# Kernel tuning notes

Hardware: AMD Instinct MI355X
Metric: run time of the kernel (lower is better)

Reference implementation:

```python
import jax, jax.numpy as jnp
import numpy as np

LAMBDA = 20.0   # lambda_val (blackbox-diff smoothing)
REG = 0.5       # reg
MAX_LABEL = 8   # labels drawn in [0, MAX_LABEL)


def _pairwise_dist(x):
    # x: [n, d] -> [n, n] euclidean distances (safe sqrt, exact 0 on diagonal)
    sq = jnp.sum(x * x, axis=-1)
    d2 = sq[:, None] + sq[None, :] - 2.0 * (x @ x.T)
    d2 = jnp.maximum(d2, 0.0)
    return jnp.where(d2 > 0, jnp.sqrt(jnp.where(d2 > 0, d2, 1.0)), 0.0)


def _single_linkage_adj(D, k):
    # Agglomerative (single-linkage) clustering of n points given [n,n] dists,
    # stopped at k clusters; returns [n,n] 0/1 cluster-adjacency matrix.
    n = D.shape[0]
    BIG = jnp.asarray(1e9, D.dtype)
    eye = jnp.eye(n, dtype=bool)
    Dw0 = jnp.where(eye, BIG, D)
    labels0 = jnp.arange(n)
    active0 = jnp.ones((n,), dtype=bool)

    def step(carry, _):
        Dw, labels, active = carry
        mask = active[:, None] & active[None, :] & ~eye
        flat = jnp.argmin(jnp.where(mask, Dw, BIG))
        i, j = flat // n, flat % n
        a = jnp.minimum(i, j)
        b = jnp.maximum(i, j)
        newrow = jnp.minimum(Dw[a], Dw[b])        # single linkage merge
        Dw = Dw.at[a, :].set(newrow).at[:, a].set(newrow)
        active = active.at[b].set(False)
        labels = jnp.where(labels == b, a, labels)
        return (Dw, labels, active), labels

    _, hist = jax.lax.scan(step, (Dw0, labels0, active0), None, length=n - 1)
    all_hist = jnp.concatenate([labels0[None, :], hist], axis=0)  # [n, n]; row m = labels after m merges (n-m clusters)
    lab = all_hist[n - k]
    return (lab[:, None] == lab[None, :]).astype(D.dtype)


def _solve(dists, ks):
    return jax.vmap(_single_linkage_adj)(dists, ks)


def setup_inputs() -> dict:
    key = jax.random.key(0)
    k1, k2, k3 = jax.random.split(key, 3)
    B, n, d = 256, 64, 768
    return {
        "query_embedding": jax.random.normal(k1, (B, d), dtype=jnp.float32),
        "psg_embeddings": jax.random.normal(k2, (B, n, d), dtype=jnp.float32),
        "labels": jax.random.randint(k3, (B, n), 0, MAX_LABEL, dtype=jnp.int64)
        if jax.config.jax_enable_x64 else jax.random.randint(k3, (B, n), 0, MAX_LABEL, dtype=jnp.int32),
    }


def reference(query_embedding, psg_embeddings, labels):
    # true_adj_mat: adj[i,j] = 1 iff i==j or label[i]==label[j] (diag is label-equal anyway)
    true_adj = (labels[:, :, None] == labels[:, None, :]).astype(jnp.float32)  # [B,n,n]
    # ks[i] = number of unique labels in sample i
    presence = (labels[..., None] == jnp.arange(MAX_LABEL)).any(axis=1)  # [B, MAX_LABEL]
    ks = presence.sum(axis=-1)

    scaled = query_embedding[:, None, :] * psg_embeddings            # [B,n,d]
    dists = jax.vmap(_pairwise_dist)(scaled)                          # [B,n,n]

    mean_similar = (dists * true_adj).sum() / true_adj.sum()
    mean_dissimilar = (dists * (1.0 - true_adj)).sum() / (1.0 - true_adj).sum()

    adj = _solve(dists, ks)                                           # OptimCluster forward
    err = adj * (1.0 - true_adj) + (1.0 - adj) * true_adj
    err_mean = err.mean(axis=0).sum()
    return err_mean + REG * (mean_similar - mean_dissimilar)
```

## Files before the change

### kernel.cpp

```cpp
#include <hip/hip_runtime.h>


#define NPTS 64
#define DIM 768
#define CH 128
#define NCH 6
#define NT 512
#define BIGF 1e9f
#define PGS 68

typedef __attribute__((ext_vector_type(8))) __bf16 bf16x8;
typedef __attribute__((ext_vector_type(4))) float f32x4;
typedef __attribute__((ext_vector_type(8))) unsigned short us8;

__device__ __forceinline__ void lds_fence() {
  asm volatile("s_waitcnt lgkmcnt(0)" ::: "memory");
  __builtin_amdgcn_sched_barrier(0);
}

__device__ __forceinline__ void split3(float x, unsigned short& h,
                                       unsigned short& m, unsigned short& l) {
  unsigned u = __float_as_uint(x);
  unsigned rb = (u + 0x7FFFu + ((u >> 16) & 1u)) & 0xFFFF0000u;
  h = (unsigned short)(rb >> 16);
  float r1 = x - __uint_as_float(rb);
  unsigned u1 = __float_as_uint(r1);
  unsigned rb1 = (u1 + 0x7FFFu + ((u1 >> 16) & 1u)) & 0xFFFF0000u;
  m = (unsigned short)(rb1 >> 16);
  float r2 = r1 - __uint_as_float(rb1);
  l = (unsigned short)(__float_as_uint(r2) >> 16);
}

__device__ __forceinline__ unsigned long long match6(int v) {
  unsigned long long m = ~0ull;
  #pragma unroll
  for (int bb = 0; bb < 6; ++bb) {
    unsigned long long mb = __ballot(((v >> bb) & 1) != 0);
    m &= (((v >> bb) & 1) != 0) ? mb : ~mb;
  }
  return m;
}

__device__ __forceinline__ void stage_chunk(
    unsigned short (*Hb)[NPTS][CH], const float4 (&pva)[2][2],
    const float4 (&qv)[2], int row0, int gran) {
  #pragma unroll
  for (int rr = 0; rr < 2; ++rr) {
    const int row = row0 + (rr << 5);
    float xs[8];
    xs[0] = pva[rr][0].x * qv[0].x; xs[1] = pva[rr][0].y * qv[0].y;
    xs[2] = pva[rr][0].z * qv[0].z; xs[3] = pva[rr][0].w * qv[0].w;
    xs[4] = pva[rr][1].x * qv[1].x; xs[5] = pva[rr][1].y * qv[1].y;
    xs[6] = pva[rr][1].z * qv[1].z; xs[7] = pva[rr][1].w * qv[1].w;
    us8 uh, um, ul;
    #pragma unroll
    for (int e = 0; e < 8; ++e) {
      unsigned short hh, mm, ll;
      split3(xs[e], hh, mm, ll);
      uh[e] = hh; um[e] = mm; ul[e] = ll;
    }
    const int p = gran ^ (row & 15);
    *reinterpret_cast<us8*>(&Hb[0][row][p << 3]) = uh;
    *reinterpret_cast<us8*>(&Hb[1][row][p << 3]) = um;
    *reinterpret_cast<us8*>(&Hb[2][row][p << 3]) = ul;
  }
}

__device__ __forceinline__ void mfma_chunk(
    const unsigned short (*Hb)[NPTS][CH], f32x4 (&acc)[2][2],
    int R, int C, int ksub, int lrow, int lhi) {
  #pragma unroll 1
  for (int ss = 0; ss < 2; ++ss) {
    const int s = ksub + (ss << 1);
    const int p = ((s << 2) + lhi) ^ lrow;
    bf16x8 fa[3][2], fb[3][2];
    #pragma unroll
    for (int v = 0; v < 3; ++v)
      #pragma unroll
      for (int tb = 0; tb < 2; ++tb) {
        const int row = (R << 5) + (tb << 4) + lrow;
        fa[v][tb] = *reinterpret_cast<const bf16x8*>(&Hb[v][row][p << 3]);
      }
    if (R != C) {
      #pragma unroll
      for (int v = 0; v < 3; ++v)
        #pragma unroll
        for (int tb = 0; tb < 2; ++tb) {
          const int row = (C << 5) + (tb << 4) + lrow;
          fb[v][tb] = *reinterpret_cast<const bf16x8*>(&Hb[v][row][p << 3]);
        }
    } else {
      #pragma unroll
      for (int v = 0; v < 3; ++v)
        #pragma unroll
        for (int tb = 0; tb < 2; ++tb) fb[v][tb] = fa[v][tb];
    }
    #pragma unroll
    for (int ti = 0; ti < 2; ++ti)
      #pragma unroll
      for (int tj = 0; tj < 2; ++tj) {
        acc[ti][tj] = __builtin_amdgcn_mfma_f32_16x16x32_bf16(fa[0][ti], fb[0][tj], acc[ti][tj], 0, 0, 0);
        acc[ti][tj] = __builtin_amdgcn_mfma_f32_16x16x32_bf16(fa[0][ti], fb[1][tj], acc[ti][tj], 0, 0, 0);
        acc[ti][tj] = __builtin_amdgcn_mfma_f32_16x16x32_bf16(fa[1][ti], fb[0][tj], acc[ti][tj], 0, 0, 0);
        acc[ti][tj] = __builtin_amdgcn_mfma_f32_16x16x32_bf16(fa[1][ti], fb[1][tj], acc[ti][tj], 0, 0, 0);
        acc[ti][tj] = __builtin_amdgcn_mfma_f32_16x16x32_bf16(fa[0][ti], fb[2][tj], acc[ti][tj], 0, 0, 0);
        acc[ti][tj] = __builtin_amdgcn_mfma_f32_16x16x32_bf16(fa[2][ti], fb[0][tj], acc[ti][tj], 0, 0, 0);
      }
  }
}

#define ISSUE_P(PV, cix) do {                                       \
    const int off_ = (cix) * CH;                                    \
    PV[0][0] = *(const float4*)(pr0 + off_);                        \
    PV[0][1] = *(const float4*)(pr0 + off_ + 4);                    \
    PV[1][0] = *(const float4*)(pr1 + off_);                        \
    PV[1][1] = *(const float4*)(pr1 + off_ + 4);                    \
  } while (0)

#define ISSUE_Q(QV, cix) do {                                       \
    const int off_ = (cix) * CH;                                    \
    QV[0] = *(const float4*)(qr + off_);                            \
    QV[1] = *(const float4*)(qr + off_ + 4);                        \
  } while (0)

__global__ __launch_bounds__(NT) void fused_kernel(
    const float* __restrict__ q,
    const float* __restrict__ psg,
    const int*   __restrict__ labels,
    float* __restrict__ simS_o, float* __restrict__ disS_o,
    int* __restrict__ simC_o, int* __restrict__ errC_o)
{
  __shared__ __align__(16) unsigned short Hml[2][3][NPTS][CH];
  __shared__ __align__(16) float PG[NPTS * PGS];
  __shared__ float diagf[NPTS];
  __shared__ unsigned bw_s[NPTS], bfl_s[NPTS];
  __shared__ int lab_s[NPTS];
  __shared__ __align__(8) unsigned long long ekey_s[NPTS];

  const int b = blockIdx.x;
  const int t = threadIdx.x;
  const int w = t >> 6;
  const int l = t & 63;

  const float* qb = q + (size_t)b * DIM;
  const float* pb = psg + (size_t)b * NPTS * DIM;

  const int row0 = t >> 4;
  const int gran = t & 15;
  const float* pr0 = pb + (size_t)row0 * DIM + (gran << 3);
  const float* pr1 = pr0 + 32 * DIM;
  const float* qr  = qb + (gran << 3);

  const int rw = w >> 1;
  const int R = rw >> 1, C = rw & 1;
  const int ksub = w & 1;
  const int lrow = l & 15;
  const int lhi  = l >> 4;

  f32x4 acc[2][2];
  {
    f32x4 z = {0.f, 0.f, 0.f, 0.f};
    acc[0][0] = z; acc[0][1] = z; acc[1][0] = z; acc[1][1] = z;
  }

  float4 pvaA[2][2], pvaB[2][2], qv[2];

  ISSUE_P(pvaA, 0);
  ISSUE_Q(qv, 0);
  ISSUE_P(pvaB, 1);
  stage_chunk(Hml[0], pvaA, qv, row0, gran);
  __syncthreads();

  #pragma unroll 1
  for (int cc = 0; cc < 3; ++cc) {
    if (cc < 2) ISSUE_P(pvaA, 2 * cc + 2);
    ISSUE_Q(qv, 2 * cc + 1);
    mfma_chunk(Hml[0], acc, R, C, ksub, lrow, lhi);
    stage_chunk(Hml[1], pvaB, qv, row0, gran);
    __syncthreads();
    if (cc < 2) {
      ISSUE_P(pvaB, 2 * cc + 3);
      ISSUE_Q(qv, 2 * cc + 2);
    }
    mfma_chunk(Hml[1], acc, R, C, ksub, lrow, lhi);
    if (cc < 2) stage_chunk(Hml[0], pvaA, qv, row0, gran);
    __syncthreads();
  }

  if (w & 1) {
    float* dst = PG + (rw << 10);
    #pragma unroll
    for (int ti = 0; ti < 2; ++ti)
      #pragma unroll
      for (int tj = 0; tj < 2; ++tj)
        *reinterpret_cast<f32x4*>(dst + (((ti << 1) + tj) << 8) + (l << 2)) = acc[ti][tj];
  }
  __syncthreads();
  if (!(w & 1)) {
    const float* src = PG + (rw << 10);
    #pragma unroll
    for (int ti = 0; ti < 2; ++ti)
      #pragma unroll
      for (int tj = 0; tj < 2; ++tj)
        acc[ti][tj] += *reinterpret_cast<const f32x4*>(src + (((ti << 1) + tj) << 8) + (l << 2));
  }
  __syncthreads();
  if (!(w & 1)) {
    #pragma unroll
    for (int ti = 0; ti < 2; ++ti)
      #pragma unroll
      for (int tj = 0; tj < 2; ++tj)
        #pragma unroll
        for (int reg = 0; reg < 4; ++reg) {
          const int grow = (R << 5) + (ti << 4) + (lhi << 2) + reg;
          const int gcol = (C << 5) + (tj << 4) + lrow;
          PG[grow * PGS + gcol] = acc[ti][tj][reg];
        }
  }
  __syncthreads();

  if (t < NPTS) diagf[t] = PG[t * PGS + t];
  __syncthreads();
  {
    const int r  = t >> 3;
    const int c0 = (t & 7) << 3;
    const float dr = diagf[r];
    #pragma unroll
    for (int e = 0; e < 8; ++e) {
      const int cc = c0 + e;
      const float gg = PG[r * PGS + cc];
      float d2 = dr + diagf[cc] - 2.f * gg;
      d2 = fmaxf(d2, 0.f);
      PG[r * PGS + cc] = (d2 > 0.f) ? sqrtf(d2) : 0.f;
    }
  }
  __syncthreads();
  if (w != 0) return;

  float drow[64];
  #pragma unroll
  for (int v4 = 0; v4 < 16; ++v4) {
    f32x4 x = *reinterpret_cast<const f32x4*>(&PG[l * PGS + (v4 << 2)]);
    drow[v4 * 4 + 0] = x[0]; drow[v4 * 4 + 1] = x[1];
    drow[v4 * 4 + 2] = x[2]; drow[v4 * 4 + 3] = x[3];
  }
  int tl = labels[b * NPTS + l];

  unsigned long long sMask = 0ull;
  int kcnt = 0;
  #pragma unroll
  for (int v = 0; v < 8; ++v) {
    unsigned long long mv = __ballot(tl == v);
    kcnt += (mv != 0ull) ? 1 : 0;
    if (tl == v) sMask = mv;
  }
  int simC = __popcll(sMask);
  const int merges = NPTS - kcnt;

  float simS = 0.f, disS = 0.f;
  #pragma unroll
  for (int j = 0; j < NPTS; ++j) {
    bool sim = (sMask >> j) & 1ull;
    simS += sim ? drow[j] : 0.f;
    disS += sim ? 0.f : drow[j];
  }

  unsigned long long same = 1ull << l;
  int repSlot = l;
  int ecnt = 0;

  #pragma unroll 1
  for (int rd = 0; rd < 6; ++rd) {
    bw_s[l] = 0xFFFFFFFFu; bfl_s[l] = 0xFFFFFFFFu;
    lds_fence();
    float bv = BIGF; int bj = 64;
    #pragma unroll
    for (int j = 0; j < NPTS; ++j) {
      bool ok = !((same >> j) & 1ull) && (drow[j] < bv);
      bv = ok ? drow[j] : bv;
      bj = ok ? j : bj;
    }
    if (bj < 64) atomicMin(&bw_s[repSlot], __float_as_uint(bv));
    lds_fence();
    const unsigned bwc = bw_s[repSlot];
    if (bj < 64 && __float_as_uint(bv) == bwc)
      atomicMin(&bfl_s[repSlot], (unsigned)((l << 6) | bj));
    lds_fence();
    const unsigned rfl = bfl_s[repSlot];
    const bool valid = (bwc != 0xFFFFFFFFu);
    const int vpt = (int)(rfl & 63);
    const int otherRep = __shfl(repSlot, vpt);
    const bool isRoot = (l == repSlot);
    int ptr = repSlot;
    if (isRoot && valid) ptr = otherRep;
    const int pd = __shfl(ptr, ptr);
    bool adder = false;
    if (isRoot && valid && ptr != l) {
      if (pd == l && l < ptr) ptr = l;
      else adder = true;
    }
    const unsigned long long A = __ballot(adder);
    if (adder)
      ekey_s[ecnt + __popcll(A & ((1ull << l) - 1ull))] =
          ((unsigned long long)bwc << 12) | (unsigned long long)rfl;
    ecnt += (int)__popcll(A);
    #pragma unroll 1
    for (int jj = 0; jj < 6; ++jj) {
      const int p2 = __shfl(ptr, ptr);
      if (__ballot(p2 != ptr) == 0ull) break;
      ptr = p2;
    }
    same = match6(ptr);
    repSlot = __ffsll((long long)same) - 1;
    if (same == ~0ull) break;
  }
  lds_fence();

  const bool ehave = (l < ecnt);
  const unsigned long long my = ehave ? ekey_s[l] : ~0ull;
  int rank = 0;
  #pragma unroll 7
  for (int j = 0; j < 63; ++j) {
    unsigned long long kj = ekey_s[j];
    rank += (j < ecnt && kj < my) ? 1 : 0;
  }
  const bool kept = ehave && (rank < merges);
  const int eu = (int)((my >> 6) & 63);
  const int ev = (int)(my & 63);

  lab_s[l] = l;
  lds_fence();
  #pragma unroll 1
  for (int iter = 0; iter < 64; ++iter) {
    int m = 0; bool ch = false;
    if (kept) {
      const int lu = lab_s[eu], lv = lab_s[ev];
      m = min(lu, lv);
      ch = (m < lu) || (m < lv);
    }
    if (ch) {
      atomicMin(&lab_s[eu], m);
      atomicMin(&lab_s[ev], m);
    }
    lds_fence();
    const int la = lab_s[l];
    const int lb = lab_s[la];
    if (lb < la) lab_s[l] = lb;
    lds_fence();
    if (__ballot(ch) == 0ull) break;
  }
  const int cl = lab_s[l];

  const unsigned long long cMask = match6(cl);
  int ec2 = __popcll(cMask ^ sMask);

  #pragma unroll
  for (int off = 32; off; off >>= 1) {
    simS += __shfl_xor(simS, off);
    disS += __shfl_xor(disS, off);
    simC += __shfl_xor(simC, off);
    ec2  += __shfl_xor(ec2, off);
  }
  if (l == 0) {
    simS_o[b] = simS; disS_o[b] = disS;
    simC_o[b] = simC; errC_o[b] = ec2;
  }
}

__global__ __launch_bounds__(64) void finalize_kernel(
    const float* __restrict__ simS, const float* __restrict__ disS,
    const int* __restrict__ simC, const int* __restrict__ errC,
    float* __restrict__ out)
{
  const int l = threadIdx.x;
  double ss = 0.0, dd = 0.0, sc = 0.0, ec = 0.0;
  #pragma unroll
  for (int r = 0; r < 4; ++r) {
    int i = (r << 6) + l;
    ss += (double)simS[i];
    dd += (double)disS[i];
    sc += (double)simC[i];
    ec += (double)errC[i];
  }
  #pragma unroll
  for (int off = 32; off; off >>= 1) {
    ss += __shfl_xor(ss, off);
    dd += __shfl_xor(dd, off);
    sc += __shfl_xor(sc, off);
    ec += __shfl_xor(ec, off);
  }
  if (l == 0) {
    const double total = 256.0 * 4096.0;
    double ms = ss / sc;
    double md = dd / (total - sc);
    out[0] = (float)(ec / 256.0 + 0.5 * (ms - md));
  }
}

extern "C" void kernel_launch(void* const* d_in, const int* in_sizes, int n_in,
                              void* d_out, int out_size, void* d_ws, size_t ws_size,
                              hipStream_t stream) {
  const float* q      = (const float*)d_in[0];
  const float* psg    = (const float*)d_in[1];
  const int*   labels = (const int*)d_in[2];
  float* out = (float*)d_out;

  float* simS = (float*)d_ws;
  float* disS = simS + 256;
  int*   simC = (int*)(disS + 256);
  int*   errC = simC + 256;

  fused_kernel<<<256, NT, 0, stream>>>(q, psg, labels, simS, disS, simC, errC);
  finalize_kernel<<<1, 64, 0, stream>>>(simS, disS, simC, errC, out);
}
```

Before: 32.13 us.

## Drop third bf16 split term and split fused kernel into gram and cluster kernels

The bf16 emulation of fp32 matmul goes from a three-way split (hi/mid/lo, six MFMAs per tile pair) to a two-way split (hi/mid, four MFMAs), cutting staging work, LDS footprint and MFMA count. The kernel is also split in two: a 512-thread gram kernel writes the distance matrices to global workspace, and a separate 64-thread kernel runs the serial clustering. This frees the big block from waiting on the single-wave clustering tail, but adds a global round trip and an extra launch. The lower precision could change argmin tie decisions in clustering.

```diff
diff --git a/kernel.cpp b/kernel.cpp
--- a/kernel.cpp
+++ b/kernel.cpp
@@ -18,8 +18,8 @@
   __builtin_amdgcn_sched_barrier(0);
 }
 
-__device__ __forceinline__ void split3(float x, unsigned short& h,
-                                       unsigned short& m, unsigned short& l) {
+__device__ __forceinline__ void split2(float x, unsigned short& h,
+                                       unsigned short& m) {
   unsigned u = __float_as_uint(x);
   unsigned rb = (u + 0x7FFFu + ((u >> 16) & 1u)) & 0xFFFF0000u;
   h = (unsigned short)(rb >> 16);
@@ -27,8 +27,6 @@
   unsigned u1 = __float_as_uint(r1);
   unsigned rb1 = (u1 + 0x7FFFu + ((u1 >> 16) & 1u)) & 0xFFFF0000u;
   m = (unsigned short)(rb1 >> 16);
-  float r2 = r1 - __uint_as_float(rb1);
-  l = (unsigned short)(__float_as_uint(r2) >> 16);
 }
 
 __device__ __forceinline__ unsigned long long match6(int v) {
@@ -52,17 +50,16 @@
     xs[2] = pva[rr][0].z * qv[0].z; xs[3] = pva[rr][0].w * qv[0].w;
     xs[4] = pva[rr][1].x * qv[1].x; xs[5] = pva[rr][1].y * qv[1].y;
     xs[6] = pva[rr][1].z * qv[1].z; xs[7] = pva[rr][1].w * qv[1].w;
-    us8 uh, um, ul;
+    us8 uh, um;
     #pragma unroll
     for (int e = 0; e < 8; ++e) {
-      unsigned short hh, mm, ll;
-      split3(xs[e], hh, mm, ll);
-      uh[e] = hh; um[e] = mm; ul[e] = ll;
+      unsigned short hh, mm;
+      split2(xs[e], hh, mm);
+      uh[e] = hh; um[e] = mm;
     }
     const int p = gran ^ (row & 15);
     *reinterpret_cast<us8*>(&Hb[0][row][p << 3]) = uh;
     *reinterpret_cast<us8*>(&Hb[1][row][p << 3]) = um;
-    *reinterpret_cast<us8*>(&Hb[2][row][p << 3]) = ul;
   }
 }
 
@@ -73,9 +70,9 @@
   for (int ss = 0; ss < 2; ++ss) {
     const int s = ksub + (ss << 1);
     const int p = ((s << 2) + lhi) ^ lrow;
-    bf16x8 fa[3][2], fb[3][2];
-    #pragma unroll
-    for (int v = 0; v < 3; ++v)
+    bf16x8 fa[2][2], fb[2][2];
+    #pragma unroll
+    for (int v = 0; v < 2; ++v)
       #pragma unroll
       for (int tb = 0; tb < 2; ++tb) {
         const int row = (R << 5) + (tb << 4) + lrow;
@@ -83,7 +80,7 @@
       }
     if (R != C) {
       #pragma unroll
-      for (int v = 0; v < 3; ++v)
+      for (int v = 0; v < 2; ++v)
         #pragma unroll
         for (int tb = 0; tb < 2; ++tb) {
           const int row = (C << 5) + (tb << 4) + lrow;
@@ -91,7 +88,7 @@
         }
     } else {
       #pragma unroll
-      for (int v = 0; v < 3; ++v)
+      for (int v = 0; v < 2; ++v)
         #pragma unroll
         for (int tb = 0; tb < 2; ++tb) fb[v][tb] = fa[v][tb];
     }
@@ -103,8 +100,6 @@
         acc[ti][tj] = __builtin_amdgcn_mfma_f32_16x16x32_bf16(fa[0][ti], fb[1][tj], acc[ti][tj], 0, 0, 0);
         acc[ti][tj] = __builtin_amdgcn_mfma_f32_16x16x32_bf16(fa[1][ti], fb[0][tj], acc[ti][tj], 0, 0, 0);
         acc[ti][tj] = __builtin_amdgcn_mfma_f32_16x16x32_bf16(fa[1][ti], fb[1][tj], acc[ti][tj], 0, 0, 0);
-        acc[ti][tj] = __builtin_amdgcn_mfma_f32_16x16x32_bf16(fa[0][ti], fb[2][tj], acc[ti][tj], 0, 0, 0);
-        acc[ti][tj] = __builtin_amdgcn_mfma_f32_16x16x32_bf16(fa[2][ti], fb[0][tj], acc[ti][tj], 0, 0, 0);
       }
   }
 }
@@ -123,19 +118,14 @@
     QV[1] = *(const float4*)(qr + off_ + 4);                        \
   } while (0)
 
-__global__ __launch_bounds__(NT) void fused_kernel(
+__global__ __launch_bounds__(NT) void gram_kernel(
     const float* __restrict__ q,
     const float* __restrict__ psg,
-    const int*   __restrict__ labels,
-    float* __restrict__ simS_o, float* __restrict__ disS_o,
-    int* __restrict__ simC_o, int* __restrict__ errC_o)
+    float* __restrict__ Dg)
 {
-  __shared__ __align__(16) unsigned short Hml[2][3][NPTS][CH];
+  __shared__ __align__(16) unsigned short Hml[2][2][NPTS][CH];
   __shared__ __align__(16) float PG[NPTS * PGS];
   __shared__ float diagf[NPTS];
-  __shared__ unsigned bw_s[NPTS], bfl_s[NPTS];
-  __shared__ int lab_s[NPTS];
-  __shared__ __align__(8) unsigned long long ekey_s[NPTS];
 
   const int b = blockIdx.x;
   const int t = threadIdx.x;
@@ -225,24 +215,41 @@
     const int r  = t >> 3;
     const int c0 = (t & 7) << 3;
     const float dr = diagf[r];
+    float vout[8];
     #pragma unroll
     for (int e = 0; e < 8; ++e) {
       const int cc = c0 + e;
       const float gg = PG[r * PGS + cc];
       float d2 = dr + diagf[cc] - 2.f * gg;
       d2 = fmaxf(d2, 0.f);
-      PG[r * PGS + cc] = (d2 > 0.f) ? sqrtf(d2) : 0.f;
-    }
-  }
-  __syncthreads();
-  if (w != 0) return;
+      vout[e] = (d2 > 0.f) ? sqrtf(d2) : 0.f;
+    }
+    float* Db = Dg + (size_t)b * NPTS * NPTS;
+    *(float4*)(Db + (r << 6) + c0)     = make_float4(vout[0], vout[1], vout[2], vout[3]);
+    *(float4*)(Db + (r << 6) + c0 + 4) = make_float4(vout[4], vout[5], vout[6], vout[7]);
+  }
+}
+
+__global__ __launch_bounds__(64) void cluster_kernel(
+    const float* __restrict__ Dg,
+    const int*   __restrict__ labels,
+    float* __restrict__ simS_o, float* __restrict__ disS_o,
+    int* __restrict__ simC_o, int* __restrict__ errC_o)
+{
+  __shared__ unsigned bw_s[NPTS], bfl_s[NPTS];
+  __shared__ int lab_s[NPTS];
+  __shared__ __align__(8) unsigned long long ekey_s[NPTS];
+
+  const int b = blockIdx.x;
+  const int l = threadIdx.x;
+  const float* Db = Dg + (size_t)b * NPTS * NPTS;
 
   float drow[64];
   #pragma unroll
   for (int v4 = 0; v4 < 16; ++v4) {
-    f32x4 x = *reinterpret_cast<const f32x4*>(&PG[l * PGS + (v4 << 2)]);
-    drow[v4 * 4 + 0] = x[0]; drow[v4 * 4 + 1] = x[1];
-    drow[v4 * 4 + 2] = x[2]; drow[v4 * 4 + 3] = x[3];
+    float4 x = *reinterpret_cast<const float4*>(Db + (l << 6) + (v4 << 2));
+    drow[v4 * 4 + 0] = x.x; drow[v4 * 4 + 1] = x.y;
+    drow[v4 * 4 + 2] = x.z; drow[v4 * 4 + 3] = x.w;
   }
   int tl = labels[b * NPTS + l];
 
@@ -405,11 +412,13 @@
   const int*   labels = (const int*)d_in[2];
   float* out = (float*)d_out;
 
-  float* simS = (float*)d_ws;
+  float* Dg   = (float*)d_ws;
+  float* simS = Dg + 256 * NPTS * NPTS;
   float* disS = simS + 256;
   int*   simC = (int*)(disS + 256);
   int*   errC = simC + 256;
 
-  fused_kernel<<<256, NT, 0, stream>>>(q, psg, labels, simS, disS, simC, errC);
+  gram_kernel<<<256, NT, 0, stream>>>(q, psg, Dg);
+  cluster_kernel<<<256, 64, 0, stream>>>(Dg, labels, simS, disS, simC, errC);
   finalize_kernel<<<1, 64, 0, stream>>>(simS, disS, simC, errC, out);
 }
```

Result: slower. 33.05 us (+2.9%).
